# Performance work log

Hardware: AMD Instinct MI355X
Metric: run time of the kernel (lower is better)

The kernel has to match this reference:

```python
import jax, jax.numpy as jnp
import numpy as np
import math

NUM_HEADS = 16  # power of two -> simple ALiBi slope formula

def alibi_slopes(num_heads: int) -> jnp.ndarray:
    # num_heads is a power of two here; general formula per Press et al. 2022
    k = 1 << (num_heads.bit_length() - 1)
    ratio = 2.0 ** (-8.0 / k)
    slopes = ratio ** np.arange(1, 1 + k)
    if num_heads != k:
        ratio2 = 2.0 ** (-8.0 / (2 * k))
        rest = (ratio2 ** np.arange(1, 1 + 2 * k, 2))[: num_heads - k]
        slopes = np.concatenate([slopes, rest])
    return jnp.asarray(slopes, dtype=jnp.float32).reshape(1, -1, 1, 1)


def setup_inputs() -> dict:
    key = jax.random.key(0)
    kq, kk, kv, km = jax.random.split(key, 4)
    B, H, S, D = 1, NUM_HEADS, 2048, 64
    query = jax.random.normal(kq, (B, H, S, D), dtype=jnp.float32)
    k_ = jax.random.normal(kk, (B, H, S, D), dtype=jnp.float32)
    value = jax.random.normal(kv, (B, H, S, D), dtype=jnp.float32)
    # padding-style boolean mask [B, S]; keep position 0 always valid
    mask = jax.random.randint(km, (B, S), 0, 2).astype(bool)
    mask = mask.at[:, 0].set(True)
    return {"query": query, "key": k_, "value": value, "mask": mask}


def reference(query, key, value, mask):
    B, H, S, D = query.shape
    scale = 1.0 / math.sqrt(D)
    # scores: [B, H, Sq, Sk]
    scores = jnp.einsum("bhqd,bhkd->bhqk", query, key) * scale
    # causal ALiBi bias: distances arange(1-S, 1) -> shape (1, H, 1, S)
    distances = jnp.arange(1 - S, 1, dtype=jnp.float32)
    bias = distances[None, None, None, :] * alibi_slopes(H)
    scores = scores + bias
    # boolean padding mask [B, S] -> [B, 1, 1, S]
    blocked = jnp.finfo(scores.dtype).min
    scores = jnp.where(mask[:, None, None, :], scores, blocked)
    weights = jax.nn.softmax(scores, axis=-1)
    # dropout_prob = 0.0 (eval) -> identity
    return jnp.einsum("bhqk,bhkd->bhqd", weights, value)
```

## Files before the change

kernel.cpp:

```cpp
#include <hip/hip_runtime.h>


constexpr int   S_LEN  = 2048;
constexpr int   D_DIM  = 64;
constexpr int   H_NUM  = 16;
constexpr int   QT     = 128;
constexpr int   K_TILE = 64;
constexpr int   NTILE  = S_LEN / K_TILE;
constexpr int   QB     = S_LEN / QT;
constexpr int   PROWSTR= 36;
constexpr float SCL    = 0.18033688f;
constexpr float L2E    = 1.44269504f;
constexpr float MASKED = -50000.0f;
constexpr float CUTOFF = 40.0f;

typedef short bf16x8 __attribute__((ext_vector_type(8)));
typedef short bf16x4 __attribute__((ext_vector_type(4)));
typedef float f32x4  __attribute__((ext_vector_type(4)));

__device__ inline short f2bf(float f) {
    union { float f; unsigned u; } x; x.f = f;
    return (short)((x.u + 0x7fffu + ((x.u >> 16) & 1u)) >> 16);
}

__device__ inline unsigned pack2bf(float a, float b) {
#if __has_builtin(__builtin_amdgcn_cvt_pk_bf16_f32)
    auto p = __builtin_amdgcn_cvt_pk_bf16_f32(a, b);
    unsigned u; __builtin_memcpy(&u, &p, 4); return u;
#else
    return (unsigned)(unsigned short)f2bf(a) | ((unsigned)(unsigned short)f2bf(b) << 16);
#endif
}

__device__ inline float fexp2(float x) {
#if __has_builtin(__builtin_amdgcn_exp2f)
    return __builtin_amdgcn_exp2f(x);
#else
    return exp2f(x);
#endif
}

__device__ inline unsigned permb(unsigned hi, unsigned lo, unsigned sel) {
#if __has_builtin(__builtin_amdgcn_perm)
    return __builtin_amdgcn_perm(hi, lo, sel);
#else
    return (sel == 0x05040100u) ? ((lo & 0xffffu) | (hi << 16))
                                : ((lo >> 16) | (hi & 0xffff0000u));
#endif
}

__device__ inline void load_lds16(const void* g, void* l) {
    __builtin_amdgcn_global_load_lds((const __attribute__((address_space(1))) void*)g,
                                     (__attribute__((address_space(3))) void*)l, 16, 0, 0);
}

__device__ inline int head_t0(int h) {
    const float slope_l2e = exp2f(-0.5f * (float)(h + 1)) * L2E;
    const float kmin = 2047.0f - CUTOFF / slope_l2e;
    return kmin <= 0.0f ? 0 : ((int)kmin) >> 6;
}

__global__ __launch_bounds__(256)
void preprocess_kernel(const float* __restrict__ Km, const float* __restrict__ Vm,
                       const void* __restrict__ maskp,
                       short* __restrict__ Kswz, short* __restrict__ Vswz,
                       float* __restrict__ Bias)
{
    __shared__ int mask_is_i32;
    const int tid = threadIdx.x;
    const int kt = blockIdx.x, h = blockIdx.y;
    if (kt < head_t0(h)) return;

    const int kbase = kt * K_TILE;
    const size_t tbase = ((size_t)h * S_LEN + kbase) * D_DIM;
    short* Kd = Kswz + ((size_t)h * NTILE + kt) * 4096;
    short* Vd = Vswz + ((size_t)h * NTILE + kt) * 4096;

    if (tid < 64) {
        const unsigned v = ((const unsigned*)maskp)[tid];
        const unsigned long long b = __ballot(v <= 1u);
        if (tid == 0) mask_is_i32 = (b == ~0ULL);
    }

    #pragma unroll
    for (int it = 0; it < 2; ++it) {
        const int idx = it * 256 + tid;
        const int key = idx >> 3, c = idx & 7;
        const float* src = Km + tbase + key * 64 + c * 8;
        float4 a = *(const float4*)src;
        float4 b = *(const float4*)(src + 4);
        unsigned u[4] = { pack2bf(a.x, a.y), pack2bf(a.z, a.w),
                          pack2bf(b.x, b.y), pack2bf(b.z, b.w) };
        bf16x8 kp; __builtin_memcpy(&kp, u, 16);
        *(bf16x8*)(Kd + key * 64 + ((c ^ (key & 7)) << 3)) = kp;
    }

    {
        const int db = tid >> 4, kb = tid & 15;
        const int d4 = db * 4, key4 = kb * 4;
        float4 vv[4];
        #pragma unroll
        for (int j = 0; j < 4; ++j)
            vv[j] = *(const float4*)(Vm + tbase + (key4 + j) * 64 + d4);
        const float* vp = (const float*)vv;
        #pragma unroll
        for (int jj = 0; jj < 4; ++jj) {
            const int d = d4 + jj;
            bf16x4 ov;
            ov[0] = f2bf(vp[0 * 4 + jj]); ov[1] = f2bf(vp[1 * 4 + jj]);
            ov[2] = f2bf(vp[2 * 4 + jj]); ov[3] = f2bf(vp[3 * 4 + jj]);
            *(bf16x4*)(Vd + d * 64 + (((key4 >> 3) ^ (d & 7)) << 3) + (key4 & 7)) = ov;
        }
    }
    __syncthreads();
    if (tid < K_TILE) {
        const int key = kbase + tid;
        const int mv = mask_is_i32 ? ((const int*)maskp)[key]
                                   : (int)((const unsigned char*)maskp)[key];
        const float slope_l2e = exp2f(-0.5f * (float)(h + 1)) * L2E;
        Bias[h * S_LEN + key] = mv ? slope_l2e * (float)(key - (S_LEN - 1)) : MASKED;
    }
}

__global__ __launch_bounds__(512, 2)
void attn_main(const float* __restrict__ Qm, const short* __restrict__ Kswz,
               const short* __restrict__ Vswz, const float* __restrict__ Bias,
               float* __restrict__ Om)
{
    __shared__ short    k_lds[2][2][4096];
    __shared__ short    v_lds[2][2][4096];
    __shared__ float    bias_lds[S_LEN / QB * QB / 1];
    __shared__ unsigned p_lds[8][32 * PROWSTR];
    __shared__ float    l_cb[4][32];

    static_assert(sizeof(bias_lds) == S_LEN * sizeof(float), "bias_lds size");

    const int tid = threadIdx.x;
    const int wave = tid >> 6, lane = tid & 63;
    const int l16 = lane & 15, quad = lane >> 4;
    const int sw = wave & 3;
    const int cw = wave >> 2;
    const int h = blockIdx.y, qblk = blockIdx.x;

    const int t0 = head_t0(h);
    const int nt = NTILE - t0;
    const int nhalf = (nt + 1) >> 1;
    const int mylen  = (cw == 0) ? nhalf : nt - nhalf;
    const int mybase = (cw == 0) ? t0 : t0 + nhalf;

    const unsigned psel = (quad < 2) ? 0x05040100u : 0x07060302u;
    const short* Kh = Kswz + (size_t)h * NTILE * 4096;
    const short* Vh = Vswz + (size_t)h * NTILE * 4096;
    unsigned* pw = p_lds[wave];
    const int swz = l16 & 7;
    const int so  = sw * 2048 + lane * 16;

    *(float4*)&bias_lds[tid * 4] = *(const float4*)(Bias + (size_t)h * S_LEN + tid * 4);
    if (mylen > 0) {
        const char* kg = (const char*)(Kh + (size_t)mybase * 4096);
        const char* vg = (const char*)(Vh + (size_t)mybase * 4096);
        char* kl = (char*)&k_lds[cw][0][0] + sw * 2048;
        char* vl = (char*)&v_lds[cw][0][0] + sw * 2048;
        load_lds16(kg + so,        kl);
        load_lds16(kg + so + 1024, kl + 1024);
        load_lds16(vg + so,        vl);
        load_lds16(vg + so + 1024, vl + 1024);
    }

    bf16x8 qfrag[2][2];
    {
        const float* Qh = Qm + (size_t)h * S_LEN * D_DIM;
        #pragma unroll
        for (int s = 0; s < 2; ++s) {
            const int qrow = qblk * QT + sw * 32 + s * 16 + l16;
            #pragma unroll
            for (int t = 0; t < 2; ++t) {
                const float* src = Qh + (size_t)qrow * D_DIM + t * 32 + quad * 8;
                float4 a = *(const float4*)src;
                float4 b = *(const float4*)(src + 4);
                unsigned* qp = (unsigned*)&qfrag[s][t];
                qp[0] = pack2bf(a.x * SCL, a.y * SCL);
                qp[1] = pack2bf(a.z * SCL, a.w * SCL);
                qp[2] = pack2bf(b.x * SCL, b.y * SCL);
                qp[3] = pack2bf(b.z * SCL, b.w * SCL);
            }
        }
    }

    bf16x8 onesv;
    #pragma unroll
    for (int i = 0; i < 8; ++i) onesv[i] = (short)0x3F80;

    f32x4 o_frag[2][4], l4[2];
    #pragma unroll
    for (int s = 0; s < 2; ++s) {
        #pragma unroll
        for (int cc = 0; cc < 4; ++cc) o_frag[s][cc] = (f32x4){0.f, 0.f, 0.f, 0.f};
        l4[s] = (f32x4){0.f, 0.f, 0.f, 0.f};
    }

    __syncthreads();

    for (int i = 0; i < nhalf; ++i) {
        const int buf = i & 1;
        if (i + 1 < mylen) {
            const int ktn = mybase + i + 1;
            const char* kg = (const char*)(Kh + (size_t)ktn * 4096);
            const char* vg = (const char*)(Vh + (size_t)ktn * 4096);
            char* kl = (char*)&k_lds[cw][buf ^ 1][0] + sw * 2048;
            char* vl = (char*)&v_lds[cw][buf ^ 1][0] + sw * 2048;
            load_lds16(kg + so,        kl);
            load_lds16(kg + so + 1024, kl + 1024);
            load_lds16(vg + so,        vl);
            load_lds16(vg + so + 1024, vl + 1024);
        }
        if (i < mylen) {
            const int kt = mybase + i;
            const float* bm = &bias_lds[kt * K_TILE];
            const short* kb = &k_lds[cw][buf][0];
            const short* vb = &v_lds[cw][buf][0];

            f32x4 sv[2][4];
            __builtin_amdgcn_s_setprio(1);
            #pragma unroll
            for (int cc = 0; cc < 4; ++cc) {
                const float b = bm[cc * 16 + l16];
                const f32x4 binit = (f32x4){b, b, b, b};
                sv[0][cc] = binit;
                sv[1][cc] = binit;
                #pragma unroll
                for (int t = 0; t < 2; ++t) {
                    bf16x8 bfrag = *(const bf16x8*)&kb[(cc * 16 + l16) * 64 + (((t * 4 + quad) ^ swz) << 3)];
                    sv[0][cc] = __builtin_amdgcn_mfma_f32_16x16x32_bf16(qfrag[0][t], bfrag, sv[0][cc], 0, 0, 0);
                    sv[1][cc] = __builtin_amdgcn_mfma_f32_16x16x32_bf16(qfrag[1][t], bfrag, sv[1][cc], 0, 0, 0);
                }
            }
            __builtin_amdgcn_s_setprio(0);

            #pragma unroll
            for (int s = 0; s < 2; ++s) {
                #pragma unroll
                for (int r = 0; r < 4; ++r) {
                    const float p0 = fexp2(sv[s][0][r]);
                    const float p1 = fexp2(sv[s][1][r]);
                    const float p2 = fexp2(sv[s][2][r]);
                    const float p3 = fexp2(sv[s][3][r]);
                    unsigned* pp = &pw[(s * 16 + quad * 4 + r) * PROWSTR + l16];
                    pp[0]  = pack2bf(p0, p1);
                    pp[16] = pack2bf(p2, p3);
                }
            }

            #pragma unroll
            for (int t2 = 0; t2 < 2; ++t2) {
                bf16x8 pfrag[2];
                #pragma unroll
                for (int s = 0; s < 2; ++s) {
                    const unsigned* pr = &pw[(s * 16 + l16) * PROWSTR + t2 * 16 + (quad & 1) * 8];
                    uint4 w0 = *(const uint4*)(pr);
                    uint4 w1 = *(const uint4*)(pr + 4);
                    unsigned pf[4];
                    pf[0] = permb(w0.y, w0.x, psel);
                    pf[1] = permb(w0.w, w0.z, psel);
                    pf[2] = permb(w1.y, w1.x, psel);
                    pf[3] = permb(w1.w, w1.z, psel);
                    __builtin_memcpy(&pfrag[s], pf, 16);
                }
                __builtin_amdgcn_s_setprio(1);
                #pragma unroll
                for (int c2 = 0; c2 < 4; ++c2) {
                    bf16x8 vfrag = *(const bf16x8*)&vb[(c2 * 16 + l16) * 64 + (((t2 * 4 + quad) ^ swz) << 3)];
                    o_frag[0][c2] = __builtin_amdgcn_mfma_f32_16x16x32_bf16(pfrag[0], vfrag, o_frag[0][c2], 0, 0, 0);
                    o_frag[1][c2] = __builtin_amdgcn_mfma_f32_16x16x32_bf16(pfrag[1], vfrag, o_frag[1][c2], 0, 0, 0);
                }
                l4[0] = __builtin_amdgcn_mfma_f32_16x16x32_bf16(pfrag[0], onesv, l4[0], 0, 0, 0);
                l4[1] = __builtin_amdgcn_mfma_f32_16x16x32_bf16(pfrag[1], onesv, l4[1], 0, 0, 0);
                __builtin_amdgcn_s_setprio(0);
            }
        }
        __syncthreads();
    }

    float* cb = (float*)p_lds;
    if (cw == 1) {
        #pragma unroll
        for (int s = 0; s < 2; ++s) {
            #pragma unroll
            for (int c2 = 0; c2 < 4; ++c2) {
                #pragma unroll
                for (int r = 0; r < 4; ++r)
                    cb[(sw * 32 + s * 16 + quad * 4 + r) * 68 + c2 * 16 + l16] = o_frag[s][c2][r];
            }
            if (l16 == 0) {
                #pragma unroll
                for (int r = 0; r < 4; ++r)
                    l_cb[sw][s * 16 + quad * 4 + r] = l4[s][r];
            }
        }
    }
    __syncthreads();
    if (cw == 0) {
        float* Oh = Om + (size_t)h * S_LEN * D_DIM;
        const int qrow0 = qblk * QT + sw * 32;
        #pragma unroll
        for (int s = 0; s < 2; ++s) {
            #pragma unroll
            for (int r = 0; r < 4; ++r) {
                const int rrow = s * 16 + quad * 4 + r;
                float lsum = l4[s][r] + l_cb[sw][rrow];
                const float inv = 1.0f / lsum;
                const int row = qrow0 + rrow;
                float* dst = Oh + (size_t)row * D_DIM + l16;
                const float* cr = &cb[(sw * 32 + rrow) * 68];
                dst[0]  = (o_frag[s][0][r] + cr[0  + l16]) * inv;
                dst[16] = (o_frag[s][1][r] + cr[16 + l16]) * inv;
                dst[32] = (o_frag[s][2][r] + cr[32 + l16]) * inv;
                dst[48] = (o_frag[s][3][r] + cr[48 + l16]) * inv;
            }
        }
    }
}

extern "C" void kernel_launch(void* const* d_in, const int* in_sizes, int n_in,
                              void* d_out, int out_size, void* d_ws, size_t ws_size,
                              hipStream_t stream) {
    (void)in_sizes; (void)n_in; (void)out_size; (void)ws_size;
    const float* Q = (const float*)d_in[0];
    const float* K = (const float*)d_in[1];
    const float* V = (const float*)d_in[2];
    const void*  M = d_in[3];
    float* O = (float*)d_out;

    char* ws = (char*)d_ws;
    size_t off = 0;
    short* Kswz = (short*)(ws + off); off += (size_t)H_NUM * S_LEN * D_DIM * 2;
    short* Vswz = (short*)(ws + off); off += (size_t)H_NUM * S_LEN * D_DIM * 2;
    float* Bias = (float*)(ws + off); off += (size_t)H_NUM * S_LEN * 4;

    preprocess_kernel<<<dim3(NTILE, H_NUM), 256, 0, stream>>>(K, V, M, Kswz, Vswz, Bias);
    attn_main<<<dim3(QB, H_NUM), 512, 0, stream>>>(Q, Kswz, Vswz, Bias, O);
}
```

Before: 109.0 us.

## Split key range across blocks per head with a separate combine kernel

Adds a third grid dimension that splits each head's active key tiles into up to four partitions, so heads with long ALiBi-visible ranges spread their work over more blocks. Partial unnormalized outputs and row sums go to workspace, and a new combine kernel sums them and normalizes. Heads needing one partition still write the output directly. The K/V LDS buffering drops from double-buffered prefetch to a single buffer with two barriers per tile, which exposes load latency. It also adds an extra kernel launch and partial-result traffic to global memory.

```diff
diff --git a/kernel.cpp b/kernel.cpp
--- a/kernel.cpp
+++ b/kernel.cpp
@@ -7,6 +7,7 @@
 constexpr int   QT     = 128;
 constexpr int   K_TILE = 64;
 constexpr int   NTILE  = S_LEN / K_TILE;
+constexpr int   NPMAX  = 4;
 constexpr int   QB     = S_LEN / QT;
 constexpr int   PROWSTR= 36;
 constexpr float SCL    = 0.18033688f;
@@ -58,6 +59,11 @@
     const float slope_l2e = exp2f(-0.5f * (float)(h + 1)) * L2E;
     const float kmin = 2047.0f - CUTOFF / slope_l2e;
     return kmin <= 0.0f ? 0 : ((int)kmin) >> 6;
+}
+__device__ inline int head_np(int h) {
+    const int nt = NTILE - head_t0(h);
+    const int np = (nt + 7) >> 3;
+    return np > NPMAX ? NPMAX : np;
 }
 
 __global__ __launch_bounds__(256)
@@ -125,28 +131,33 @@
 __global__ __launch_bounds__(512, 2)
 void attn_main(const float* __restrict__ Qm, const short* __restrict__ Kswz,
                const short* __restrict__ Vswz, const float* __restrict__ Bias,
-               float* __restrict__ Om)
+               float* __restrict__ Om, float* __restrict__ Opart,
+               float* __restrict__ lp)
 {
-    __shared__ short    k_lds[2][2][4096];
-    __shared__ short    v_lds[2][2][4096];
-    __shared__ float    bias_lds[S_LEN / QB * QB / 1];
+    __shared__ short    k_lds[2][4096];
+    __shared__ short    v_lds[2][4096];
+    __shared__ float    bias_lds[512];
     __shared__ unsigned p_lds[8][32 * PROWSTR];
     __shared__ float    l_cb[4][32];
-
-    static_assert(sizeof(bias_lds) == S_LEN * sizeof(float), "bias_lds size");
 
     const int tid = threadIdx.x;
     const int wave = tid >> 6, lane = tid & 63;
     const int l16 = lane & 15, quad = lane >> 4;
     const int sw = wave & 3;
     const int cw = wave >> 2;
-    const int h = blockIdx.y, qblk = blockIdx.x;
-
+    const int h = blockIdx.y, qblk = blockIdx.x, p = blockIdx.z;
+
+    const int np = head_np(h);
+    if (p >= np) return;
     const int t0 = head_t0(h);
     const int nt = NTILE - t0;
-    const int nhalf = (nt + 1) >> 1;
-    const int mylen  = (cw == 0) ? nhalf : nt - nhalf;
-    const int mybase = (cw == 0) ? t0 : t0 + nhalf;
+    const int tstart = t0 + (p * nt) / np;
+    const int tend   = t0 + ((p + 1) * nt) / np;
+    const int glen   = tend - tstart;
+    const int half0  = (glen + 1) >> 1;
+    const int mylen  = cw ? glen - half0 : half0;
+    const int mybase = tstart + (cw ? half0 : 0);
+    const int gmax   = half0;
 
     const unsigned psel = (quad < 2) ? 0x05040100u : 0x07060302u;
     const short* Kh = Kswz + (size_t)h * NTILE * 4096;
@@ -155,16 +166,10 @@
     const int swz = l16 & 7;
     const int so  = sw * 2048 + lane * 16;
 
-    *(float4*)&bias_lds[tid * 4] = *(const float4*)(Bias + (size_t)h * S_LEN + tid * 4);
-    if (mylen > 0) {
-        const char* kg = (const char*)(Kh + (size_t)mybase * 4096);
-        const char* vg = (const char*)(Vh + (size_t)mybase * 4096);
-        char* kl = (char*)&k_lds[cw][0][0] + sw * 2048;
-        char* vl = (char*)&v_lds[cw][0][0] + sw * 2048;
-        load_lds16(kg + so,        kl);
-        load_lds16(kg + so + 1024, kl + 1024);
-        load_lds16(vg + so,        vl);
-        load_lds16(vg + so + 1024, vl + 1024);
+    {
+        const int tt = tid >> 6, kk = tid & 63;
+        if (tstart + tt < tend)
+            bias_lds[tid] = Bias[(size_t)h * S_LEN + (tstart + tt) * K_TILE + kk];
     }
 
     bf16x8 qfrag[2][2];
@@ -199,26 +204,25 @@
         l4[s] = (f32x4){0.f, 0.f, 0.f, 0.f};
     }
 
-    __syncthreads();
-
-    for (int i = 0; i < nhalf; ++i) {
-        const int buf = i & 1;
-        if (i + 1 < mylen) {
-            const int ktn = mybase + i + 1;
-            const char* kg = (const char*)(Kh + (size_t)ktn * 4096);
-            const char* vg = (const char*)(Vh + (size_t)ktn * 4096);
-            char* kl = (char*)&k_lds[cw][buf ^ 1][0] + sw * 2048;
-            char* vl = (char*)&v_lds[cw][buf ^ 1][0] + sw * 2048;
+    for (int i = 0; i < gmax; ++i) {
+        __syncthreads();
+        if (i < mylen) {
+            const int kt = mybase + i;
+            const char* kg = (const char*)(Kh + (size_t)kt * 4096);
+            const char* vg = (const char*)(Vh + (size_t)kt * 4096);
+            char* kl = (char*)&k_lds[cw][0] + sw * 2048;
+            char* vl = (char*)&v_lds[cw][0] + sw * 2048;
             load_lds16(kg + so,        kl);
             load_lds16(kg + so + 1024, kl + 1024);
             load_lds16(vg + so,        vl);
             load_lds16(vg + so + 1024, vl + 1024);
         }
+        __syncthreads();
         if (i < mylen) {
             const int kt = mybase + i;
-            const float* bm = &bias_lds[kt * K_TILE];
-            const short* kb = &k_lds[cw][buf][0];
-            const short* vb = &v_lds[cw][buf][0];
+            const float* bm = &bias_lds[(kt - tstart) * K_TILE];
+            const short* kb = &k_lds[cw][0];
+            const short* vb = &v_lds[cw][0];
 
             f32x4 sv[2][4];
             __builtin_amdgcn_s_setprio(1);
@@ -278,8 +282,8 @@
                 __builtin_amdgcn_s_setprio(0);
             }
         }
-        __syncthreads();
-    }
+    }
+    __syncthreads();
 
     float* cb = (float*)p_lds;
     if (cw == 1) {
@@ -300,25 +304,69 @@
     }
     __syncthreads();
     if (cw == 0) {
-        float* Oh = Om + (size_t)h * S_LEN * D_DIM;
-        const int qrow0 = qblk * QT + sw * 32;
-        #pragma unroll
-        for (int s = 0; s < 2; ++s) {
-            #pragma unroll
-            for (int r = 0; r < 4; ++r) {
-                const int rrow = s * 16 + quad * 4 + r;
-                float lsum = l4[s][r] + l_cb[sw][rrow];
-                const float inv = 1.0f / lsum;
-                const int row = qrow0 + rrow;
-                float* dst = Oh + (size_t)row * D_DIM + l16;
-                const float* cr = &cb[(sw * 32 + rrow) * 68];
-                dst[0]  = (o_frag[s][0][r] + cr[0  + l16]) * inv;
-                dst[16] = (o_frag[s][1][r] + cr[16 + l16]) * inv;
-                dst[32] = (o_frag[s][2][r] + cr[32 + l16]) * inv;
-                dst[48] = (o_frag[s][3][r] + cr[48 + l16]) * inv;
-            }
-        }
-    }
+        if (np == 1) {
+            float* Oh = Om + (size_t)h * S_LEN * D_DIM;
+            const int qrow0 = qblk * QT + sw * 32;
+            #pragma unroll
+            for (int s = 0; s < 2; ++s) {
+                #pragma unroll
+                for (int r = 0; r < 4; ++r) {
+                    const int rrow = s * 16 + quad * 4 + r;
+                    const float inv = 1.0f / (l4[s][r] + l_cb[sw][rrow]);
+                    const float* cr = &cb[(sw * 32 + rrow) * 68];
+                    float* dst = Oh + (size_t)(qrow0 + rrow) * D_DIM + l16;
+                    dst[0]  = (o_frag[s][0][r] + cr[0  + l16]) * inv;
+                    dst[16] = (o_frag[s][1][r] + cr[16 + l16]) * inv;
+                    dst[32] = (o_frag[s][2][r] + cr[32 + l16]) * inv;
+                    dst[48] = (o_frag[s][3][r] + cr[48 + l16]) * inv;
+                }
+            }
+        } else {
+            #pragma unroll
+            for (int s = 0; s < 2; ++s) {
+                const int g = qblk * 32 + sw * 8 + s * 4 + quad;
+                const size_t gbase = (((size_t)h * NPMAX + p) * 512 + g);
+                f32x4 lsum;
+                #pragma unroll
+                for (int r = 0; r < 4; ++r)
+                    lsum[r] = l4[s][r] + l_cb[sw][s * 16 + quad * 4 + r];
+                #pragma unroll
+                for (int c2 = 0; c2 < 4; ++c2) {
+                    f32x4 ov;
+                    #pragma unroll
+                    for (int r = 0; r < 4; ++r)
+                        ov[r] = o_frag[s][c2][r] + cb[(sw * 32 + s * 16 + quad * 4 + r) * 68 + c2 * 16 + l16];
+                    *(f32x4*)(Opart + (gbase * 64 + c2 * 16 + l16) * 4) = ov;
+                }
+                if (l16 == 0) *(f32x4*)(lp + gbase * 4) = lsum;
+            }
+        }
+    }
+}
+
+__global__ __launch_bounds__(256)
+void attn_combine_kernel(const float* __restrict__ Opart, const float* __restrict__ lp,
+                         float* __restrict__ Om)
+{
+    const int t   = blockIdx.x * 256 + threadIdx.x;
+    const int col = t & 63;
+    const int g   = (t >> 6) & 511;
+    const int h   = t >> 15;
+
+    const int np = head_np(h);
+    if (np == 1) return;
+
+    f32x4 acc = (f32x4){0.f, 0.f, 0.f, 0.f};
+    f32x4 den = (f32x4){0.f, 0.f, 0.f, 0.f};
+    for (int c = 0; c < np; ++c) {
+        const size_t gbase = (((size_t)h * NPMAX + c) * 512 + g);
+        den += *(const f32x4*)(lp + gbase * 4);
+        acc += *(const f32x4*)(Opart + (gbase * 64 + col) * 4);
+    }
+    float* Oh = Om + (size_t)h * S_LEN * D_DIM;
+    #pragma unroll
+    for (int r = 0; r < 4; ++r)
+        Oh[(size_t)(g * 4 + r) * 64 + col] = acc[r] / den[r];
 }
 
 extern "C" void kernel_launch(void* const* d_in, const int* in_sizes, int n_in,
@@ -336,7 +384,10 @@
     short* Kswz = (short*)(ws + off); off += (size_t)H_NUM * S_LEN * D_DIM * 2;
     short* Vswz = (short*)(ws + off); off += (size_t)H_NUM * S_LEN * D_DIM * 2;
     float* Bias = (float*)(ws + off); off += (size_t)H_NUM * S_LEN * 4;
+    float* Opart = (float*)(ws + off); off += (size_t)H_NUM * NPMAX * 512 * 64 * 4 * 4;
+    float* lp   = (float*)(ws + off); off += (size_t)H_NUM * NPMAX * 512 * 4 * 4;
 
     preprocess_kernel<<<dim3(NTILE, H_NUM), 256, 0, stream>>>(K, V, M, Kswz, Vswz, Bias);
-    attn_main<<<dim3(QB, H_NUM), 512, 0, stream>>>(Q, Kswz, Vswz, Bias, O);
-}
+    attn_main<<<dim3(QB, H_NUM, NPMAX), 512, 0, stream>>>(Q, Kswz, Vswz, Bias, O, Opart, lp);
+    attn_combine_kernel<<<(H_NUM * 512 * 64) / 256, 256, 0, stream>>>(Opart, lp, O);
+}
```

After: 101.4 us. -7.0%, faster.
